# Kernel optimization log

Measured on AMD Instinct MI355X. Metric: run time of the kernel, lower is better.

Reference implementation:

```python
import jax, jax.numpy as jnp
from jax import lax
import numpy as np

L, I, H, O = 8192, 256, 2048, 1


def setup_inputs() -> dict:
    key = jax.random.key(0)
    ks = jax.random.split(key, 11)
    s = 1.0 / np.sqrt(H)  # PyTorch nn.RNN init scale, keeps tanh unsaturated
    return {
        "x": jax.random.normal(ks[0], (1, L, I), dtype=jnp.float32),
        "W_ih0": jax.random.normal(ks[1], (H, I), dtype=jnp.float32) * s,
        "W_hh0": jax.random.normal(ks[2], (H, H), dtype=jnp.float32) * s,
        "b_ih0": jax.random.normal(ks[3], (H,), dtype=jnp.float32) * s,
        "b_hh0": jax.random.normal(ks[4], (H,), dtype=jnp.float32) * s,
        "W_ih1": jax.random.normal(ks[5], (H, H), dtype=jnp.float32) * s,
        "W_hh1": jax.random.normal(ks[6], (H, H), dtype=jnp.float32) * s,
        "b_ih1": jax.random.normal(ks[7], (H,), dtype=jnp.float32) * s,
        "b_hh1": jax.random.normal(ks[8], (H,), dtype=jnp.float32) * s,
        "W_fc": jax.random.normal(ks[9], (O, H), dtype=jnp.float32) * s,
        "b_fc": jax.random.normal(ks[10], (O,), dtype=jnp.float32) * s,
    }


def _rnn_layer(seq, W_ih, W_hh, b_ih, b_hh):
    # seq: [L, D_in] -> [L, H]; h_t = tanh(x_t W_ih^T + b_ih + h_{t-1} W_hh^T + b_hh)
    pre = seq @ W_ih.T + (b_ih + b_hh)  # hoist the input GEMM out of the scan

    def step(h, p):
        h = jnp.tanh(p + h @ W_hh.T)
        return h, h

    h0 = jnp.zeros((W_hh.shape[0],), dtype=seq.dtype)
    _, out = lax.scan(step, h0, pre)
    return out


def reference(x, W_ih0, W_hh0, b_ih0, b_hh0, W_ih1, W_hh1, b_ih1, b_hh1, W_fc, b_fc):
    seq = x[0]  # batch is fixed to 1 in the original module
    seq = _rnn_layer(seq, W_ih0, W_hh0, b_ih0, b_hh0)  # layer 0: [L, H]
    seq = _rnn_layer(seq, W_ih1, W_hh1, b_ih1, b_hh1)  # layer 1: [L, H]
    last = seq[-1]  # out[:, -1, :]
    out = jax.nn.sigmoid(last @ W_fc.T + b_fc)  # [O]
    return out[None, :]  # [1, O]


if __name__ == "__main__":
    inp = setup_inputs()
    print(reference(**inp).shape)
```

## Files before the change

kernel.cpp:

```cpp
#include <hip/hip_runtime.h>
#include <math.h>

#define L_SEQ 8192
#define I_DIM 256
#define H_DIM 2048
#define NWG0  64
#define NWG1  128
#define NWG   (NWG0 + NWG1)
#define TPB   512
#define RD    16
#define RM    (RD - 1)
#define TLAG  11


typedef float f32x4 __attribute__((ext_vector_type(4)));
typedef float f32x2 __attribute__((ext_vector_type(2)));

__device__ __forceinline__ void cstore1(float* p, float v) {
  asm volatile("global_store_dword %0, %1, off sc0 sc1" :: "v"(p), "v"(v) : "memory");
}
__device__ __forceinline__ void cstore2f(float* p, float a, float b) {
  f32x2 v; v.x = a; v.y = b;
  asm volatile("global_store_dwordx2 %0, %1, off sc0 sc1" :: "v"(p), "v"(v) : "memory");
}
__device__ __forceinline__ void cstore4f(float* p, float a, float b, float c, float d) {
  f32x4 v; v.x = a; v.y = b; v.z = c; v.w = d;
  asm volatile("global_store_dwordx4 %0, %1, off sc0 sc1" :: "v"(p), "v"(v) : "memory");
}
__device__ __forceinline__ void cstoreu(unsigned* p, unsigned v) {
  asm volatile("global_store_dword %0, %1, off sc0 sc1" :: "v"(p), "v"(v) : "memory");
}
__device__ __forceinline__ float cload1(const float* p) {
  float v;
  asm volatile("global_load_dword %0, %1, off sc0 sc1\n\ts_waitcnt vmcnt(0)"
               : "=v"(v) : "v"(p) : "memory");
  return v;
}
__device__ __forceinline__ unsigned cloadu(const unsigned* p) {
  unsigned v;
  asm volatile("global_load_dword %0, %1, off sc0 sc1\n\ts_waitcnt vmcnt(0)"
               : "=v"(v) : "v"(p) : "memory");
  return v;
}
__device__ __forceinline__ float4 cload4(const float* p) {
  float4 v;
  asm volatile("global_load_dwordx4 %0, %1, off sc0 sc1\n\ts_waitcnt vmcnt(0)"
               : "=v"(v) : "v"(p) : "memory");
  return v;
}
__device__ __forceinline__ float4 ld4(const float* p) {
  float4 v;
  asm volatile("global_load_dwordx4 %0, %1, off\n\ts_waitcnt vmcnt(0)"
               : "=v"(v) : "v"(p) : "memory");
  return v;
}
__device__ __forceinline__ void pf_issue(f32x4& v, const float* p) {
  asm volatile("global_load_dwordx4 %0, %1, off sc0 sc1" : "=&v"(v) : "v"(p) : "memory");
}
__device__ __forceinline__ void pf_wait(f32x4& v) {
  asm volatile("s_waitcnt vmcnt(1)" : "+v"(v) :: "memory");
  __builtin_amdgcn_sched_barrier(0);
}
__device__ __forceinline__ float tagc(int step) {
  return 4.f + 8.f * (float)((step >> 4) & 1);
}
__device__ __forceinline__ bool ok4(float4 v, float c) {
  return __builtin_fabsf(v.x - c) <= 1.f && __builtin_fabsf(v.y - c) <= 1.f &&
         __builtin_fabsf(v.z - c) <= 1.f && __builtin_fabsf(v.w - c) <= 1.f;
}
__device__ __forceinline__ bool ok4x(f32x4 v, float c) {
  return __builtin_fabsf(v.x - c) <= 1.f && __builtin_fabsf(v.y - c) <= 1.f &&
         __builtin_fabsf(v.z - c) <= 1.f && __builtin_fabsf(v.w - c) <= 1.f;
}
__device__ __forceinline__ float4 poll4(const float* p, float c) {
  float4 v = cload4(p);
  while (!ok4(v, c)) { __builtin_amdgcn_s_sleep(1); v = cload4(p); }
  return make_float4(v.x - c, v.y - c, v.z - c, v.w - c);
}
__device__ __forceinline__ float tanh_fast(float v) {
  float e = __expf(2.f * v);
  return 1.f - 2.f / (e + 1.f);
}
__device__ __forceinline__ void start_barrier(unsigned* bslots, int wg, int tid, unsigned value) {
  __syncthreads();
  if (tid == 0) cstoreu(&bslots[wg], value);
  if (tid < NWG) {
    while ((int)(cloadu(&bslots[tid]) - value) < 0) __builtin_amdgcn_s_sleep(1);
  }
  __syncthreads();
}

__global__ __launch_bounds__(TPB, 2)
void rnn2_pfetch(const float* __restrict__ x,
                 const float* __restrict__ Wih0, const float* __restrict__ Whh0,
                 const float* __restrict__ bih0, const float* __restrict__ bhh0,
                 const float* __restrict__ Wih1, const float* __restrict__ Whh1,
                 const float* __restrict__ bih1, const float* __restrict__ bhh1,
                 const float* __restrict__ Wfc,  const float* __restrict__ bfc,
                 float* __restrict__ out,
                 unsigned* __restrict__ runctr, unsigned* __restrict__ bslots,
                 float* __restrict__ h0s, float* __restrict__ h1s)
{
  const int wg  = blockIdx.x;
  const int tid = threadIdx.x;
  const int wv  = tid >> 6;
  __shared__ float4 lds4[2][1024];

  const unsigned runbase = cloadu(runctr);

  if (wg < NWG0) {
    const int cg  = tid & 15;
    const int row = wg * 32 + (tid >> 4);
    float4 wihr[4], whhr[32];
    {
      const float* wr = Wih0 + (size_t)row * I_DIM + (cg << 2);
      #pragma unroll
      for (int k = 0; k < 4; ++k) wihr[k] = ld4(wr + (k << 6));
      const float* wr2 = Whh0 + (size_t)row * H_DIM + (cg << 2);
      #pragma unroll
      for (int k = 0; k < 32; ++k) whhr[k] = ld4(wr2 + (k << 6));
    }
    const float bias = bih0[row] + bhh0[row];

    {
      int sl = tid >> 5; int r = wg * 32 + (tid & 31);
      cstore1(&h0s[sl * H_DIM + r], (sl == 0) ? 4.f : 0.f);
    }
    start_barrier(bslots, wg, tid, runbase + 1);

    float xpart = 0.f;
    #pragma unroll
    for (int k = 0; k < 4; ++k) {
      float4 xv = ((const float4*)x)[cg + 16 * k];
      xpart += wihr[k].x * xv.x + wihr[k].y * xv.y + wihr[k].z * xv.z + wihr[k].w * xv.w;
    }

    for (int s = 1; s <= L_SEQ; ++s) {
      const int P = s & 1;
      float4 hv = poll4(h0s + ((s - 1) & RM) * H_DIM + (tid << 2), tagc(s - 1));
      lds4[P][tid] = hv;
      if ((s & 3) == 0 && s >= 12 && tid < NWG1) {
        const float c = tagc(s - TLAG);
        const float* tp = h1s + ((s - TLAG) & RM) * H_DIM + (tid << 4);
        while (__builtin_fabsf(cload1(tp) - c) > 1.f) __builtin_amdgcn_s_sleep(1);
      }
      __syncthreads();
      float acc = xpart;
      #pragma unroll
      for (int k = 0; k < 32; ++k) {
        float4 h = lds4[P][cg + 16 * k];
        acc += whhr[k].x * h.x + whhr[k].y * h.y + whhr[k].z * h.z + whhr[k].w * h.w;
      }
      acc += __shfl_xor(acc, 1);
      acc += __shfl_xor(acc, 2);
      acc += __shfl_xor(acc, 4);
      acc += __shfl_xor(acc, 8);
      float hval = tanh_fast(acc + bias) + tagc(s);
      float g1 = __shfl(hval, 16);
      float g2 = __shfl(hval, 32);
      float g3 = __shfl(hval, 48);
      if ((tid & 63) == 0)
        cstore4f(h0s + (s & RM) * H_DIM + wg * 32 + wv * 4, hval, g1, g2, g3);
      if (s < L_SEQ) {
        xpart = 0.f;
        #pragma unroll
        for (int k = 0; k < 4; ++k) {
          float4 xv = ((const float4*)x)[s * 64 + cg + 16 * k];
          xpart += wihr[k].x * xv.x + wihr[k].y * xv.y + wihr[k].z * xv.z + wihr[k].w * xv.w;
        }
      }
    }

    if (wg == 0) {
      float4 hv = poll4(h1s + (tid << 2), tagc(L_SEQ));
      float4 wf = ((const float4*)Wfc)[tid];
      float pz = hv.x * wf.x + hv.y * wf.y + hv.z * wf.z + hv.w * wf.w;
      #pragma unroll
      for (int m = 1; m < 64; m <<= 1) pz += __shfl_xor(pz, m);
      float* red = (float*)&lds4[0][0];
      __syncthreads();
      if ((tid & 63) == 0) red[wv] = pz;
      __syncthreads();
      if (tid == 0) {
        float z = bfc[0];
        #pragma unroll
        for (int w = 0; w < 8; ++w) z += red[w];
        out[0] = 1.f / (1.f + __expf(-z));
        cstoreu(runctr, runbase + 1);
      }
    }
  } else {
    const int cg  = tid & 31;
    const int wgl = wg - NWG0;
    const int row = wgl * 16 + (tid >> 5);
    float4 wihr[16], whhr[16];
    {
      const float* wr = Wih1 + (size_t)row * H_DIM + (cg << 2);
      #pragma unroll
      for (int k = 0; k < 16; ++k) wihr[k] = ld4(wr + (k << 7));
      const float* wr2 = Whh1 + (size_t)row * H_DIM + (cg << 2);
      #pragma unroll
      for (int k = 0; k < 16; ++k) whhr[k] = ld4(wr2 + (k << 7));
    }
    const float bias = bih1[row] + bhh1[row];

    if (tid < 256) {
      int sl = tid >> 4; int r = wgl * 16 + (tid & 15);
      cstore1(&h1s[sl * H_DIM + r], (sl == 0) ? 4.f : 0.f);
    }
    start_barrier(bslots, wg, tid, runbase + 1);

    f32x4 pf;
    pf_issue(pf, h0s + (1 & RM) * H_DIM + (tid << 2));
    (void)cloadu(runctr);

    for (int t = 1; t <= L_SEQ; ++t) {
      const int P = t & 1;
      const float c0 = tagc(t);
      pf_wait(pf);
      if (!ok4x(pf, c0)) {
        const float* p0 = h0s + (t & RM) * H_DIM + (tid << 2);
        do {
          __builtin_amdgcn_s_sleep(1);
          float4 r = cload4(p0);
          pf.x = r.x; pf.y = r.y; pf.z = r.z; pf.w = r.w;
        } while (!ok4x(pf, c0));
      }
      lds4[P][tid] = make_float4(pf.x - c0, pf.y - c0, pf.z - c0, pf.w - c0);
      if (t < L_SEQ)
        pf_issue(pf, h0s + ((t + 1) & RM) * H_DIM + (tid << 2));
      __syncthreads();
      float acc = 0.f;
      #pragma unroll
      for (int k = 0; k < 16; ++k) {
        float4 h = lds4[P][cg + 32 * k];
        acc += wihr[k].x * h.x + wihr[k].y * h.y + wihr[k].z * h.z + wihr[k].w * h.w;
      }
      float4 b = poll4(h1s + ((t - 1) & RM) * H_DIM + (tid << 2), tagc(t - 1));
      lds4[P][512 + tid] = b;
      __syncthreads();
      #pragma unroll
      for (int k = 0; k < 16; ++k) {
        float4 h = lds4[P][512 + cg + 32 * k];
        acc += whhr[k].x * h.x + whhr[k].y * h.y + whhr[k].z * h.z + whhr[k].w * h.w;
      }
      acc += __shfl_xor(acc, 1);
      acc += __shfl_xor(acc, 2);
      acc += __shfl_xor(acc, 4);
      acc += __shfl_xor(acc, 8);
      acc += __shfl_xor(acc, 16);
      float hval = tanh_fast(acc + bias) + tagc(t);
      float g1 = __shfl(hval, 32);
      if ((tid & 63) == 0)
        cstore2f(h1s + (t & RM) * H_DIM + wgl * 16 + wv * 2, hval, g1);
    }
  }
}

extern "C" void kernel_launch(void* const* d_in, const int* in_sizes, int n_in,
                              void* d_out, int out_size, void* d_ws, size_t ws_size,
                              hipStream_t stream) {
  const float* xx   = (const float*)d_in[0];
  const float* Wih0 = (const float*)d_in[1];
  const float* Whh0 = (const float*)d_in[2];
  const float* bih0 = (const float*)d_in[3];
  const float* bhh0 = (const float*)d_in[4];
  const float* Wih1 = (const float*)d_in[5];
  const float* Whh1 = (const float*)d_in[6];
  const float* bih1 = (const float*)d_in[7];
  const float* bhh1 = (const float*)d_in[8];
  const float* Wfc  = (const float*)d_in[9];
  const float* bfc  = (const float*)d_in[10];

  unsigned* runctr = (unsigned*)d_ws;
  unsigned* bslots = (unsigned*)((char*)d_ws + 256);
  float* h0s       = (float*)((char*)d_ws + 4096);
  float* h1s       = (float*)((char*)d_ws + 4096 + RD * H_DIM * sizeof(float));

  rnn2_pfetch<<<dim3(NWG), dim3(TPB), 0, stream>>>(
      xx, Wih0, Whh0, bih0, bhh0, Wih1, Whh1, bih1, bhh1, Wfc, bfc,
      (float*)d_out, runctr, bslots, h0s, h1s);
}
```

Measured before the change: 23.23 ms.

## Give each wave whole rows with contiguous column blocks and padded LDS

Measured after the change: 18.94 ms (median of 2 runs). 1.23x faster.

```diff
diff --git a/kernel.cpp b/kernel.cpp
--- a/kernel.cpp
+++ b/kernel.cpp
@@ -57,7 +57,7 @@
 __device__ __forceinline__ void pf_issue(f32x4& v, const float* p) {
   asm volatile("global_load_dwordx4 %0, %1, off sc0 sc1" : "=&v"(v) : "v"(p) : "memory");
 }
-__device__ __forceinline__ void pf_wait(f32x4& v) {
+__device__ __forceinline__ void pf_wait1(f32x4& v) {
   asm volatile("s_waitcnt vmcnt(1)" : "+v"(v) :: "memory");
   __builtin_amdgcn_sched_barrier(0);
 }
@@ -76,6 +76,19 @@
   float4 v = cload4(p);
   while (!ok4(v, c)) { __builtin_amdgcn_s_sleep(1); v = cload4(p); }
   return make_float4(v.x - c, v.y - c, v.z - c, v.w - c);
+}
+__device__ __forceinline__ float4 pf_finish(f32x4 pf, const float* p, float c) {
+  if (!ok4x(pf, c)) {
+    do {
+      __builtin_amdgcn_s_sleep(1);
+      float4 r = cload4(p);
+      pf.x = r.x; pf.y = r.y; pf.z = r.z; pf.w = r.w;
+    } while (!ok4x(pf, c));
+  }
+  return make_float4(pf.x - c, pf.y - c, pf.z - c, pf.w - c);
+}
+__device__ __forceinline__ float dot4(float4 a, float4 b) {
+  return a.x * b.x + a.y * b.y + a.z * b.z + a.w * b.w;
 }
 __device__ __forceinline__ float tanh_fast(float v) {
   float e = __expf(2.f * v);
@@ -91,36 +104,41 @@
 }
 
 __global__ __launch_bounds__(TPB, 2)
-void rnn2_pfetch(const float* __restrict__ x,
-                 const float* __restrict__ Wih0, const float* __restrict__ Whh0,
-                 const float* __restrict__ bih0, const float* __restrict__ bhh0,
-                 const float* __restrict__ Wih1, const float* __restrict__ Whh1,
-                 const float* __restrict__ bih1, const float* __restrict__ bhh1,
-                 const float* __restrict__ Wfc,  const float* __restrict__ bfc,
-                 float* __restrict__ out,
-                 unsigned* __restrict__ runctr, unsigned* __restrict__ bslots,
-                 float* __restrict__ h0s, float* __restrict__ h1s)
+void rnn2_colb(const float* __restrict__ x,
+               const float* __restrict__ Wih0, const float* __restrict__ Whh0,
+               const float* __restrict__ bih0, const float* __restrict__ bhh0,
+               const float* __restrict__ Wih1, const float* __restrict__ Whh1,
+               const float* __restrict__ bih1, const float* __restrict__ bhh1,
+               const float* __restrict__ Wfc,  const float* __restrict__ bfc,
+               float* __restrict__ out,
+               unsigned* __restrict__ runctr, unsigned* __restrict__ bslots,
+               float* __restrict__ h0s, float* __restrict__ h1s)
 {
-  const int wg  = blockIdx.x;
-  const int tid = threadIdx.x;
-  const int wv  = tid >> 6;
-  __shared__ float4 lds4[2][1024];
+  const int wg   = blockIdx.x;
+  const int tid  = threadIdx.x;
+  const int lane = tid & 63;
+  const int wv   = tid >> 6;
+  __shared__ float4 lds4[2][1152];
 
   const unsigned runbase = cloadu(runctr);
 
   if (wg < NWG0) {
-    const int cg  = tid & 15;
-    const int row = wg * 32 + (tid >> 4);
-    float4 wihr[4], whhr[32];
+    const int r0 = wg * 32 + wv * 4;
+    float4 whhr[32];
+    float4 wihr[4];
     {
-      const float* wr = Wih0 + (size_t)row * I_DIM + (cg << 2);
-      #pragma unroll
-      for (int k = 0; k < 4; ++k) wihr[k] = ld4(wr + (k << 6));
-      const float* wr2 = Whh0 + (size_t)row * H_DIM + (cg << 2);
-      #pragma unroll
-      for (int k = 0; k < 32; ++k) whhr[k] = ld4(wr2 + (k << 6));
-    }
-    const float bias = bih0[row] + bhh0[row];
+      #pragma unroll
+      for (int j = 0; j < 4; ++j) {
+        const float* wr2 = Whh0 + (size_t)(r0 + j) * H_DIM + (lane << 5);
+        #pragma unroll
+        for (int k = 0; k < 8; ++k) whhr[j * 8 + k] = ld4(wr2 + (k << 2));
+        wihr[j] = ld4(Wih0 + (size_t)(r0 + j) * I_DIM + (lane << 2));
+      }
+    }
+    const float bs0 = bih0[r0] + bhh0[r0];
+    const float bs1 = bih0[r0 + 1] + bhh0[r0 + 1];
+    const float bs2 = bih0[r0 + 2] + bhh0[r0 + 2];
+    const float bs3 = bih0[r0 + 3] + bhh0[r0 + 3];
 
     {
       int sl = tid >> 5; int r = wg * 32 + (tid & 31);
@@ -128,53 +146,54 @@
     }
     start_barrier(bslots, wg, tid, runbase + 1);
 
-    float xpart = 0.f;
-    #pragma unroll
-    for (int k = 0; k < 4; ++k) {
-      float4 xv = ((const float4*)x)[cg + 16 * k];
-      xpart += wihr[k].x * xv.x + wihr[k].y * xv.y + wihr[k].z * xv.z + wihr[k].w * xv.w;
+    float xp0, xp1, xp2, xp3;
+    {
+      float4 xv = ((const float4*)x)[lane];
+      xp0 = dot4(wihr[0], xv); xp1 = dot4(wihr[1], xv);
+      xp2 = dot4(wihr[2], xv); xp3 = dot4(wihr[3], xv);
     }
 
     for (int s = 1; s <= L_SEQ; ++s) {
       const int P = s & 1;
       float4 hv = poll4(h0s + ((s - 1) & RM) * H_DIM + (tid << 2), tagc(s - 1));
-      lds4[P][tid] = hv;
+      lds4[P][tid + (tid >> 3)] = hv;
       if ((s & 3) == 0 && s >= 12 && tid < NWG1) {
-        const float c = tagc(s - TLAG);
+        const float tc = tagc(s - TLAG);
         const float* tp = h1s + ((s - TLAG) & RM) * H_DIM + (tid << 4);
-        while (__builtin_fabsf(cload1(tp) - c) > 1.f) __builtin_amdgcn_s_sleep(1);
-      }
-      __syncthreads();
-      float acc = xpart;
-      #pragma unroll
-      for (int k = 0; k < 32; ++k) {
-        float4 h = lds4[P][cg + 16 * k];
-        acc += whhr[k].x * h.x + whhr[k].y * h.y + whhr[k].z * h.z + whhr[k].w * h.w;
-      }
-      acc += __shfl_xor(acc, 1);
-      acc += __shfl_xor(acc, 2);
-      acc += __shfl_xor(acc, 4);
-      acc += __shfl_xor(acc, 8);
-      float hval = tanh_fast(acc + bias) + tagc(s);
-      float g1 = __shfl(hval, 16);
-      float g2 = __shfl(hval, 32);
-      float g3 = __shfl(hval, 48);
-      if ((tid & 63) == 0)
-        cstore4f(h0s + (s & RM) * H_DIM + wg * 32 + wv * 4, hval, g1, g2, g3);
+        while (__builtin_fabsf(cload1(tp) - tc) > 1.f) __builtin_amdgcn_s_sleep(1);
+      }
+      __syncthreads();
+      float p0 = xp0, p1 = xp1, p2 = xp2, p3 = xp3;
+      #pragma unroll
+      for (int k = 0; k < 8; ++k) {
+        float4 h = lds4[P][9 * lane + k];
+        p0 += dot4(whhr[k], h);
+        p1 += dot4(whhr[8 + k], h);
+        p2 += dot4(whhr[16 + k], h);
+        p3 += dot4(whhr[24 + k], h);
+      }
+      #pragma unroll
+      for (int m = 1; m < 64; m <<= 1) {
+        p0 += __shfl_xor(p0, m); p1 += __shfl_xor(p1, m);
+        p2 += __shfl_xor(p2, m); p3 += __shfl_xor(p3, m);
+      }
+      if (lane == 0) {
+        const float ct = tagc(s);
+        cstore4f(h0s + (s & RM) * H_DIM + r0,
+                 tanh_fast(p0 + bs0) + ct, tanh_fast(p1 + bs1) + ct,
+                 tanh_fast(p2 + bs2) + ct, tanh_fast(p3 + bs3) + ct);
+      }
       if (s < L_SEQ) {
-        xpart = 0.f;
-        #pragma unroll
-        for (int k = 0; k < 4; ++k) {
-          float4 xv = ((const float4*)x)[s * 64 + cg + 16 * k];
-          xpart += wihr[k].x * xv.x + wihr[k].y * xv.y + wihr[k].z * xv.z + wihr[k].w * xv.w;
-        }
+        float4 xv = ((const float4*)x)[s * 64 + lane];
+        xp0 = dot4(wihr[0], xv); xp1 = dot4(wihr[1], xv);
+        xp2 = dot4(wihr[2], xv); xp3 = dot4(wihr[3], xv);
       }
     }
 
     if (wg == 0) {
       float4 hv = poll4(h1s + (tid << 2), tagc(L_SEQ));
       float4 wf = ((const float4*)Wfc)[tid];
-      float pz = hv.x * wf.x + hv.y * wf.y + hv.z * wf.z + hv.w * wf.w;
+      float pz = dot4(hv, wf);
       #pragma unroll
       for (int m = 1; m < 64; m <<= 1) pz += __shfl_xor(pz, m);
       float* red = (float*)&lds4[0][0];
@@ -190,19 +209,22 @@
       }
     }
   } else {
-    const int cg  = tid & 31;
     const int wgl = wg - NWG0;
-    const int row = wgl * 16 + (tid >> 5);
+    const int r0  = wgl * 16 + wv * 2;
     float4 wihr[16], whhr[16];
     {
-      const float* wr = Wih1 + (size_t)row * H_DIM + (cg << 2);
-      #pragma unroll
-      for (int k = 0; k < 16; ++k) wihr[k] = ld4(wr + (k << 7));
-      const float* wr2 = Whh1 + (size_t)row * H_DIM + (cg << 2);
-      #pragma unroll
-      for (int k = 0; k < 16; ++k) whhr[k] = ld4(wr2 + (k << 7));
-    }
-    const float bias = bih1[row] + bhh1[row];
+      #pragma unroll
+      for (int j = 0; j < 2; ++j) {
+        const float* wr = Wih1 + (size_t)(r0 + j) * H_DIM + (lane << 5);
+        #pragma unroll
+        for (int k = 0; k < 8; ++k) wihr[j * 8 + k] = ld4(wr + (k << 2));
+        const float* wr2 = Whh1 + (size_t)(r0 + j) * H_DIM + (lane << 5);
+        #pragma unroll
+        for (int k = 0; k < 8; ++k) whhr[j * 8 + k] = ld4(wr2 + (k << 2));
+      }
+    }
+    const float ba = bih1[r0] + bhh1[r0];
+    const float bb = bih1[r0 + 1] + bhh1[r0 + 1];
 
     if (tid < 256) {
       int sl = tid >> 4; int r = wgl * 16 + (tid & 15);
@@ -210,49 +232,44 @@
     }
     start_barrier(bslots, wg, tid, runbase + 1);
 
-    f32x4 pf;
-    pf_issue(pf, h0s + (1 & RM) * H_DIM + (tid << 2));
+    f32x4 pfA;
+    pf_issue(pfA, h0s + (1 & RM) * H_DIM + (tid << 2));
     (void)cloadu(runctr);
 
     for (int t = 1; t <= L_SEQ; ++t) {
       const int P = t & 1;
       const float c0 = tagc(t);
-      pf_wait(pf);
-      if (!ok4x(pf, c0)) {
-        const float* p0 = h0s + (t & RM) * H_DIM + (tid << 2);
-        do {
-          __builtin_amdgcn_s_sleep(1);
-          float4 r = cload4(p0);
-          pf.x = r.x; pf.y = r.y; pf.z = r.z; pf.w = r.w;
-        } while (!ok4x(pf, c0));
-      }
-      lds4[P][tid] = make_float4(pf.x - c0, pf.y - c0, pf.z - c0, pf.w - c0);
+      pf_wait1(pfA);
+      float4 a = pf_finish(pfA, h0s + (t & RM) * H_DIM + (tid << 2), c0);
+      lds4[P][tid + (tid >> 3)] = a;
       if (t < L_SEQ)
-        pf_issue(pf, h0s + ((t + 1) & RM) * H_DIM + (tid << 2));
-      __syncthreads();
-      float acc = 0.f;
-      #pragma unroll
-      for (int k = 0; k < 16; ++k) {
-        float4 h = lds4[P][cg + 32 * k];
-        acc += wihr[k].x * h.x + wihr[k].y * h.y + wihr[k].z * h.z + wihr[k].w * h.w;
+        pf_issue(pfA, h0s + ((t + 1) & RM) * H_DIM + (tid << 2));
+      __syncthreads();
+      float pa = 0.f, pb = 0.f;
+      #pragma unroll
+      for (int k = 0; k < 8; ++k) {
+        float4 h = lds4[P][9 * lane + k];
+        pa += dot4(wihr[k], h);
+        pb += dot4(wihr[8 + k], h);
       }
       float4 b = poll4(h1s + ((t - 1) & RM) * H_DIM + (tid << 2), tagc(t - 1));
-      lds4[P][512 + tid] = b;
-      __syncthreads();
-      #pragma unroll
-      for (int k = 0; k < 16; ++k) {
-        float4 h = lds4[P][512 + cg + 32 * k];
-        acc += whhr[k].x * h.x + whhr[k].y * h.y + whhr[k].z * h.z + whhr[k].w * h.w;
-      }
-      acc += __shfl_xor(acc, 1);
-      acc += __shfl_xor(acc, 2);
-      acc += __shfl_xor(acc, 4);
-      acc += __shfl_xor(acc, 8);
-      acc += __shfl_xor(acc, 16);
-      float hval = tanh_fast(acc + bias) + tagc(t);
-      float g1 = __shfl(hval, 32);
-      if ((tid & 63) == 0)
-        cstore2f(h1s + (t & RM) * H_DIM + wgl * 16 + wv * 2, hval, g1);
+      lds4[P][576 + tid + (tid >> 3)] = b;
+      __syncthreads();
+      #pragma unroll
+      for (int k = 0; k < 8; ++k) {
+        float4 h = lds4[P][576 + 9 * lane + k];
+        pa += dot4(whhr[k], h);
+        pb += dot4(whhr[8 + k], h);
+      }
+      #pragma unroll
+      for (int m = 1; m < 64; m <<= 1) {
+        pa += __shfl_xor(pa, m); pb += __shfl_xor(pb, m);
+      }
+      if (lane == 0) {
+        const float ct = tagc(t);
+        cstore2f(h1s + (t & RM) * H_DIM + r0,
+                 tanh_fast(pa + ba) + ct, tanh_fast(pb + bb) + ct);
+      }
     }
   }
 }
@@ -277,7 +294,7 @@
   float* h0s       = (float*)((char*)d_ws + 4096);
   float* h1s       = (float*)((char*)d_ws + 4096 + RD * H_DIM * sizeof(float));
 
-  rnn2_pfetch<<<dim3(NWG), dim3(TPB), 0, stream>>>(
+  rnn2_colb<<<dim3(NWG), dim3(TPB), 0, stream>>>(
       xx, Wih0, Whh0, bih0, bhh0, Wih1, Whh1, bih1, bhh1, Wfc, bfc,
       (float*)d_out, runctr, bslots, h0s, h1s);
 }
```
